# Kernel tuning notes

Hardware: AMD Instinct MI355X
Metric: run time of the kernel (lower is better)

Reference implementation:

```python
import jax, jax.numpy as jnp
import numpy as np

N, E, K = 50000, 1_000_000, 512
C, HALF, L, HID, NT = 64, 32, 16, 1024, 11
EPS = 1e-5


def _bn(x, gamma, beta):
    # BatchNorm1d in training mode: biased batch stats over node axis
    m = x.mean(axis=0)
    v = x.var(axis=0)
    return gamma * (x - m) * jax.lax.rsqrt(v + EPS) + beta


def _biconv(x, src, dst, w, n):
    # adjacency @ x  ->  out_i = sum_{(j->i) in edges} x_j  (edge (src=j, dst=i))
    out = jax.ops.segment_sum(x[src], dst, num_segments=n) @ w[0]
    # adjacency_t @ x -> scatter along src
    back = jax.ops.segment_sum(x[dst], src, num_segments=n) @ w[1]
    return jnp.concatenate([out, back], axis=1)  # [n, C]


def setup_inputs() -> dict:
    key = jax.random.key(0)
    ks = jax.random.split(key, 12)
    return {
        "node_types": jax.random.randint(ks[0], (N,), 0, NT, dtype=jnp.int32),
        "edge_index": jax.random.randint(ks[1], (2, E), 0, N, dtype=jnp.int32),
        "indices": jax.random.randint(ks[2], (K,), 0, N, dtype=jnp.int32),
        "emb": jax.random.normal(ks[3], (NT, C), dtype=jnp.float32),
        "conv0_w": jax.random.normal(ks[4], (2, C, HALF), dtype=jnp.float32) * 0.18,
        "res_bn_gamma": jnp.ones((L, 2, C), dtype=jnp.float32),
        "res_bn_beta": jnp.zeros((L, 2, C), dtype=jnp.float32),
        "res_w": jax.random.normal(ks[5], (L, 2, 2, C, HALF), dtype=jnp.float32) * 0.18,
        "hidden_w": jax.random.normal(ks[6], (18 * C, HID), dtype=jnp.float32) * 0.03,
        "hidden_b": jnp.zeros((HID,), dtype=jnp.float32),
        "out_w": jax.random.normal(ks[7], (HID, 1), dtype=jnp.float32) * 0.03,
        "out_b": jnp.zeros((1,), dtype=jnp.float32),
    }


def reference(node_types, edge_index, indices, emb, conv0_w, res_bn_gamma,
              res_bn_beta, res_w, hidden_w, hidden_b, out_w, out_b):
    n = node_types.shape[0]
    src, dst = edge_index[0], edge_index[1]

    x = emb[node_types]                       # [N, C] embedding lookup
    log0 = x
    x = _biconv(x, src, dst, conv0_w, n)      # conv0
    log1 = x

    def step(x, p):
        gamma, beta, w = p                    # [2,C], [2,C], [2,2,C,HALF]
        skip = x
        h = _bn(jax.nn.relu(x), gamma[0], beta[0])
        h = _biconv(h, src, dst, w[0], n)
        h = _bn(jax.nn.relu(h), gamma[1], beta[1])
        h = _biconv(h, src, dst, w[1], n)
        x = skip + h
        return x, x

    _, ys = jax.lax.scan(step, x, (res_bn_gamma, res_bn_beta, res_w))  # ys [L,N,C]

    full = jnp.concatenate(
        [log0, log1, ys.transpose(1, 0, 2).reshape(n, L * C)], axis=1)  # [N, 18*C]
    sel = full[indices]                        # [K, 18*C]
    h = jax.nn.relu(sel) @ hidden_w + hidden_b
    o = (jax.nn.relu(h) @ out_w + out_b).squeeze(-1)  # [K]
    return jax.nn.softmax(o, axis=0)
```

## Files before the change

### kernel.cpp

```cpp
#include <hip/hip_runtime.h>
#include <hip/hip_bf16.h>

#define NN 50000
#define NE 1000000
#define CC 64
#define LL 16
#define KSEL 512
#define HIDD 1024
#define FULLW 1152
#define EPSV 1e-5f


__global__ __launch_bounds__(256) void hist_kernel(const int* __restrict__ src,
    const int* __restrict__ dst, int* __restrict__ cnt_in, int* __restrict__ cnt_out) {
  int stride = gridDim.x * blockDim.x;
  for (int e = blockIdx.x * blockDim.x + threadIdx.x; e < NE; e += stride) {
    atomicAdd(&cnt_in[dst[e]], 1);
    atomicAdd(&cnt_out[src[e]], 1);
  }
}

__global__ __launch_bounds__(1024) void scan_kernel(const int* __restrict__ cnt,
    int* __restrict__ rp) {
  const int* c = cnt + blockIdx.x * NN;
  int* r = rp + blockIdx.x * (NN + 1);
  __shared__ int part[1024];
  int t = threadIdx.x;
  const int CH = (NN + 1023) / 1024;
  int beg = t * CH;
  int end = min(beg + CH, NN);
  int s = 0;
  for (int i = beg; i < end; ++i) s += c[i];
  part[t] = s;
  __syncthreads();
  if (t == 0) {
    int run = 0;
    for (int i = 0; i < 1024; ++i) { int v = part[i]; part[i] = run; run += v; }
  }
  __syncthreads();
  int off = part[t];
  for (int i = beg; i < end; ++i) { r[i] = off; off += c[i]; }
  if (t == 1023) r[NN] = off;
}

__global__ __launch_bounds__(256) void initcur_kernel(const int* __restrict__ rp_in,
    const int* __restrict__ rp_out, int* __restrict__ cur_in, int* __restrict__ cur_out,
    float* __restrict__ statsA) {
  int i = blockIdx.x * 256 + threadIdx.x;
  if (i < NN) cur_in[i] = rp_in[i];
  else if (i < 2 * NN) cur_out[i - NN] = rp_out[i - NN];
  if (blockIdx.x == 0 && threadIdx.x < 128) statsA[threadIdx.x] = 0.f;
}

__global__ __launch_bounds__(256) void fill_kernel(const int* __restrict__ src,
    const int* __restrict__ dst, int* __restrict__ cur_in, int* __restrict__ cur_out,
    int* __restrict__ col_in, int* __restrict__ col_out) {
  int stride = gridDim.x * blockDim.x;
  for (int e = blockIdx.x * blockDim.x + threadIdx.x; e < NE; e += stride) {
    int s = src[e], d = dst[e];
    int p = atomicAdd(&cur_in[d], 1);
    col_in[p] = s;
    int q = atomicAdd(&cur_out[s], 1);
    col_out[q] = d;
  }
}


__global__ __launch_bounds__(256) void embed_kernel(const int* __restrict__ nt,
    const float* __restrict__ emb, float* __restrict__ X) {
  int id = blockIdx.x * 256 + threadIdx.x;
  if (id >= NN * CC) return;
  X[id] = emb[nt[id >> 6] * CC + (id & 63)];
}

__global__ __launch_bounds__(256) void gather_sel_kernel(const float* __restrict__ xsrc,
    const int* __restrict__ idx, float* __restrict__ sel, int coloff) {
  int tid = blockIdx.x * 256 + threadIdx.x;
  if (tid >= KSEL * CC) return;
  int k = tid >> 6, cch = tid & 63;
  sel[k * FULLW + coloff + cch] = xsrc[idx[k] * CC + cch];
}


__global__ __launch_bounds__(256) void mm_kernel(const float* __restrict__ X,
    __hip_bfloat16* __restrict__ Y, const float* __restrict__ W,
    const float* __restrict__ stats, const float* __restrict__ gamma,
    const float* __restrict__ beta, float* __restrict__ stats_zero) {
  int t = threadIdx.x;
  int lane = t & 63;
  int wid = t >> 6;
  float wreg[CC];
  {
    const float* wb = W + (lane >> 5) * 2048 + (lane & 31);
#pragma unroll
    for (int c2 = 0; c2 < CC; ++c2) wreg[c2] = wb[c2 * 32];
  }
  __shared__ float sc[CC], sh[CC];
  __shared__ __align__(16) float Xs[64][CC];
  if (t < CC) {
    float scale = 1.f, shift = 0.f;
    if (stats) {
      float m = stats[t] * (1.f / NN);
      float v = stats[CC + t] * (1.f / NN) - m * m;
      float is = rsqrtf(v + EPSV);
      scale = gamma[t] * is;
      shift = beta[t] - m * scale;
    }
    sc[t] = scale; sh[t] = shift;
  }
  if (stats_zero && blockIdx.x == 0 && t < 128) stats_zero[t] = 0.f;
  const bool bn = (stats != nullptr);
  for (int row0 = blockIdx.x * 64; row0 < NN; row0 += gridDim.x * 64) {
    int nrows = min(64, NN - row0);
    __syncthreads();
    for (int idx = t; idx < nrows * CC; idx += 256) {
      int r = idx >> 6, cch = idx & 63;
      float v = X[(row0 + r) * CC + cch];
      if (bn) { v = fmaxf(v, 0.f); v = v * sc[cch] + sh[cch]; }
      Xs[r][cch] = v;
    }
    __syncthreads();
    for (int r = wid; r < nrows; r += 4) {
      const float* xr = &Xs[r][0];
      float a0 = 0.f, a1 = 0.f, a2 = 0.f, a3 = 0.f;
#pragma unroll
      for (int c2 = 0; c2 < CC; c2 += 4) {
        float4 xv = *(const float4*)(xr + c2);
        a0 += xv.x * wreg[c2];
        a1 += xv.y * wreg[c2 + 1];
        a2 += xv.z * wreg[c2 + 2];
        a3 += xv.w * wreg[c2 + 3];
      }
      Y[(row0 + r) * CC + lane] = __float2bfloat16((a0 + a1) + (a2 + a3));
    }
  }
}


__global__ __launch_bounds__(256) void seg_kernel(
    const __hip_bfloat16* __restrict__ Y, const float* skip, float* OUT,
    const int* __restrict__ rp_in, const int* __restrict__ col_in,
    const int* __restrict__ rp_out, const int* __restrict__ col_out,
    float* __restrict__ stats_acc) {
  int t = threadIdx.x;
  int c = t & 63;
  int local = t >> 6;
  const int* rp = (c < 32) ? rp_in : rp_out;
  const int* col = (c < 32) ? col_in : col_out;
  float s1 = 0.f, s2 = 0.f;
  for (int i0 = blockIdx.x * 4; i0 < NN; i0 += gridDim.x * 4) {
    int i = i0 + local;
    if (i < NN) {
      int beg = rp[i], end = rp[i + 1];
      float a0 = 0.f, a1 = 0.f, a2 = 0.f, a3 = 0.f;
      float a4 = 0.f, a5 = 0.f, a6 = 0.f, a7 = 0.f;
      int e = beg;
      for (; e + 8 <= end; e += 8) {
        int j0 = col[e], j1 = col[e + 1], j2 = col[e + 2], j3 = col[e + 3];
        int j4 = col[e + 4], j5 = col[e + 5], j6 = col[e + 6], j7 = col[e + 7];
        a0 += __bfloat162float(Y[j0 * CC + c]);
        a1 += __bfloat162float(Y[j1 * CC + c]);
        a2 += __bfloat162float(Y[j2 * CC + c]);
        a3 += __bfloat162float(Y[j3 * CC + c]);
        a4 += __bfloat162float(Y[j4 * CC + c]);
        a5 += __bfloat162float(Y[j5 * CC + c]);
        a6 += __bfloat162float(Y[j6 * CC + c]);
        a7 += __bfloat162float(Y[j7 * CC + c]);
      }
      if (e + 4 <= end) {
        int j0 = col[e], j1 = col[e + 1], j2 = col[e + 2], j3 = col[e + 3];
        a0 += __bfloat162float(Y[j0 * CC + c]);
        a1 += __bfloat162float(Y[j1 * CC + c]);
        a2 += __bfloat162float(Y[j2 * CC + c]);
        a3 += __bfloat162float(Y[j3 * CC + c]);
        e += 4;
      }
      if (e + 2 <= end) {
        int j0 = col[e], j1 = col[e + 1];
        a4 += __bfloat162float(Y[j0 * CC + c]);
        a5 += __bfloat162float(Y[j1 * CC + c]);
        e += 2;
      }
      if (e < end) a6 += __bfloat162float(Y[col[e] * CC + c]);
      float acc = ((a0 + a1) + (a2 + a3)) + ((a4 + a5) + (a6 + a7));
      if (skip) acc += skip[i * CC + c];
      OUT[i * CC + c] = acc;
      float r = fmaxf(acc, 0.f);
      s1 += r; s2 += r * r;
    }
  }
  if (stats_acc) {
    __shared__ float red1[256], red2[256];
    red1[t] = s1; red2[t] = s2;
    __syncthreads();
    if (t < 64) {
      float v1 = red1[t] + red1[t + 64] + red1[t + 128] + red1[t + 192];
      float v2 = red2[t] + red2[t + 64] + red2[t + 128] + red2[t + 192];
      atomicAdd(&stats_acc[t], v1);
      atomicAdd(&stats_acc[CC + t], v2);
    }
  }
}


__global__ __launch_bounds__(64) void hidden_kernel(const float* __restrict__ sel,
    const float* __restrict__ Wh, const float* __restrict__ bh, float* __restrict__ h1) {
  int lane = threadIdx.x;
  int rb = blockIdx.x & 63;
  int jb = blockIdx.x >> 6;
  int j = jb * 64 + lane;
  int r0 = rb * 8;
  float acc[8];
#pragma unroll
  for (int r = 0; r < 8; ++r) acc[r] = 0.f;
  __shared__ __align__(16) float Ss[8][64];
  for (int k0 = 0; k0 < FULLW; k0 += 64) {
    float wreg[64];
#pragma unroll
    for (int c2 = 0; c2 < 64; ++c2) wreg[c2] = Wh[(k0 + c2) * HIDD + j];
    __syncthreads();
#pragma unroll
    for (int r = 0; r < 8; ++r) {
      float v = sel[(r0 + r) * FULLW + k0 + lane];
      Ss[r][lane] = fmaxf(v, 0.f);
    }
    __syncthreads();
#pragma unroll
    for (int r = 0; r < 8; ++r) {
      const float* sr = &Ss[r][0];
      float a0 = 0.f, a1 = 0.f, a2 = 0.f, a3 = 0.f;
#pragma unroll
      for (int c2 = 0; c2 < 64; c2 += 4) {
        float4 sv = *(const float4*)(sr + c2);
        a0 += sv.x * wreg[c2]; a1 += sv.y * wreg[c2 + 1];
        a2 += sv.z * wreg[c2 + 2]; a3 += sv.w * wreg[c2 + 3];
      }
      acc[r] += (a0 + a1) + (a2 + a3);
    }
  }
#pragma unroll
  for (int r = 0; r < 8; ++r) h1[(r0 + r) * HIDD + j] = acc[r] + bh[j];
}

__global__ __launch_bounds__(256) void out_kernel(const float* __restrict__ h1,
    const float* __restrict__ ow, const float* __restrict__ ob, float* __restrict__ logits) {
  int k = blockIdx.x * 4 + (threadIdx.x >> 6);
  int lane = threadIdx.x & 63;
  if (k >= KSEL) return;
  float a = 0.f;
  for (int j = lane; j < HIDD; j += 64) {
    float v = h1[k * HIDD + j];
    a += fmaxf(v, 0.f) * ow[j];
  }
  for (int off = 32; off; off >>= 1) a += __shfl_down(a, off, 64);
  if (lane == 0) logits[k] = a + ob[0];
}

__global__ __launch_bounds__(512) void softmax_kernel(const float* __restrict__ logits,
    float* __restrict__ out) {
  int t = threadIdx.x;
  float v = logits[t];
  __shared__ float red[512];
  red[t] = v;
  __syncthreads();
  for (int s = 256; s; s >>= 1) { if (t < s) red[t] = fmaxf(red[t], red[t + s]); __syncthreads(); }
  float mx = red[0];
  __syncthreads();
  float e = expf(v - mx);
  red[t] = e;
  __syncthreads();
  for (int s = 256; s; s >>= 1) { if (t < s) red[t] += red[t + s]; __syncthreads(); }
  out[t] = e / red[0];
}


extern "C" void kernel_launch(void* const* d_in, const int* in_sizes, int n_in,
                              void* d_out, int out_size, void* d_ws, size_t ws_size,
                              hipStream_t stream) {
  const int* node_types = (const int*)d_in[0];
  const int* edge_index = (const int*)d_in[1];
  const int* indices = (const int*)d_in[2];
  const float* emb = (const float*)d_in[3];
  const float* conv0_w = (const float*)d_in[4];
  const float* bn_g = (const float*)d_in[5];
  const float* bn_b = (const float*)d_in[6];
  const float* res_w = (const float*)d_in[7];
  const float* hw = (const float*)d_in[8];
  const float* hb = (const float*)d_in[9];
  const float* ow = (const float*)d_in[10];
  const float* ob = (const float*)d_in[11];
  float* out = (float*)d_out;
  const int* src = edge_index;
  const int* dst = edge_index + NE;

  char* p = (char*)d_ws;
  size_t off = 0;
  auto alloc = [&](size_t bytes) -> void* {
    void* q = p + off;
    off += (bytes + 255) & ~(size_t)255;
    return q;
  };
  int* cnt = (int*)alloc(2 * NN * sizeof(int));
  int* rp = (int*)alloc(2 * (NN + 1) * sizeof(int));
  int* cur = (int*)alloc(2 * NN * sizeof(int));
  int* col_in = (int*)alloc((size_t)NE * sizeof(int));
  int* col_out = (int*)alloc((size_t)NE * sizeof(int));
  float* X = (float*)alloc((size_t)NN * CC * 4);
  float* H = (float*)alloc((size_t)NN * CC * 4);
  __hip_bfloat16* Y = (__hip_bfloat16*)alloc((size_t)NN * CC * 2);
  float* statsA = (float*)alloc(128 * 4);
  float* statsB = (float*)alloc(128 * 4);
  float* sel = (float*)alloc((size_t)KSEL * FULLW * 4);
  float* h1 = (float*)alloc((size_t)KSEL * HIDD * 4);
  float* logits = (float*)alloc(KSEL * 4);
  (void)ws_size; (void)in_sizes; (void)n_in; (void)out_size;

  int* cnt_in = cnt;  int* cnt_out = cnt + NN;
  int* rp_in = rp;    int* rp_out = rp + NN + 1;
  int* cur_in = cur;  int* cur_out = cur + NN;

  hipMemsetAsync(cnt, 0, 2 * NN * sizeof(int), stream);
  hipLaunchKernelGGL(hist_kernel, dim3(1024), dim3(256), 0, stream, src, dst, cnt_in, cnt_out);
  hipLaunchKernelGGL(scan_kernel, dim3(2), dim3(1024), 0, stream, cnt, rp);
  hipLaunchKernelGGL(initcur_kernel, dim3((2 * NN + 255) / 256), dim3(256), 0, stream,
                     rp_in, rp_out, cur_in, cur_out, statsA);
  hipLaunchKernelGGL(fill_kernel, dim3(1024), dim3(256), 0, stream, src, dst,
                     cur_in, cur_out, col_in, col_out);

  hipLaunchKernelGGL(embed_kernel, dim3((NN * CC + 255) / 256), dim3(256), 0, stream,
                     node_types, emb, X);
  hipLaunchKernelGGL(gather_sel_kernel, dim3(KSEL * CC / 256), dim3(256), 0, stream,
                     X, indices, sel, 0);

  hipLaunchKernelGGL(mm_kernel, dim3(782), dim3(256), 0, stream, X, Y, conv0_w,
                     (const float*)nullptr, (const float*)nullptr, (const float*)nullptr,
                     (float*)nullptr);
  hipLaunchKernelGGL(seg_kernel, dim3(2048), dim3(256), 0, stream, Y, (const float*)nullptr, X,
                     rp_in, col_in, rp_out, col_out, statsA);
  hipLaunchKernelGGL(gather_sel_kernel, dim3(KSEL * CC / 256), dim3(256), 0, stream,
                     X, indices, sel, CC);

  for (int l = 0; l < LL; ++l) {
    const float* w1 = res_w + (size_t)(l * 2 + 0) * 4096;
    const float* w2 = res_w + (size_t)(l * 2 + 1) * 4096;
    const float* g1 = bn_g + (l * 2 + 0) * CC;
    const float* b1 = bn_b + (l * 2 + 0) * CC;
    const float* g2 = bn_g + (l * 2 + 1) * CC;
    const float* b2 = bn_b + (l * 2 + 1) * CC;
    hipLaunchKernelGGL(mm_kernel, dim3(782), dim3(256), 0, stream, X, Y, w1, statsA, g1, b1, statsB);
    hipLaunchKernelGGL(seg_kernel, dim3(2048), dim3(256), 0, stream, Y, (const float*)nullptr, H,
                       rp_in, col_in, rp_out, col_out, statsB);
    hipLaunchKernelGGL(mm_kernel, dim3(782), dim3(256), 0, stream, H, Y, w2, statsB, g2, b2, statsA);
    hipLaunchKernelGGL(seg_kernel, dim3(2048), dim3(256), 0, stream, Y, X, X,
                       rp_in, col_in, rp_out, col_out, statsA);
    hipLaunchKernelGGL(gather_sel_kernel, dim3(KSEL * CC / 256), dim3(256), 0, stream,
                       X, indices, sel, 2 * CC + l * CC);
  }

  hipLaunchKernelGGL(hidden_kernel, dim3(1024), dim3(64), 0, stream, sel, hw, hb, h1);
  hipLaunchKernelGGL(out_kernel, dim3(KSEL / 4), dim3(256), 0, stream, h1, ow, ob, logits);
  hipLaunchKernelGGL(softmax_kernel, dim3(1), dim3(512), 0, stream, logits, out);
}
```

Before: 4.035 ms.

## Parallelize CSR prefix scan, vectorize mm loads, tile hidden layer weights in LDS

Replaces the two-block serial prefix scan with a three-stage multi-block scan that also initializes the cursor array, removing a largely sequential setup kernel. The mm kernel now loads and normalizes input rows as float4 instead of scalars. The hidden-layer kernel uses 256-thread blocks that stage weight and selected-row tiles in shared memory with coalesced float4 loads, replacing the strided per-thread global weight reads. It adds two kernel launches and a temporary buffer in exchange.

Result: faster. 3.677 ms (-8.9%).

```diff
diff --git a/kernel.cpp b/kernel.cpp
--- a/kernel.cpp
+++ b/kernel.cpp
@@ -9,6 +9,7 @@
 #define HIDD 1024
 #define FULLW 1152
 #define EPSV 1e-5f
+#define SBLK 49
 
 
 __global__ __launch_bounds__(256) void hist_kernel(const int* __restrict__ src,
@@ -20,36 +21,57 @@
   }
 }
 
-__global__ __launch_bounds__(1024) void scan_kernel(const int* __restrict__ cnt,
-    int* __restrict__ rp) {
-  const int* c = cnt + blockIdx.x * NN;
-  int* r = rp + blockIdx.x * (NN + 1);
-  __shared__ int part[1024];
-  int t = threadIdx.x;
-  const int CH = (NN + 1023) / 1024;
-  int beg = t * CH;
-  int end = min(beg + CH, NN);
-  int s = 0;
-  for (int i = beg; i < end; ++i) s += c[i];
-  part[t] = s;
+
+__global__ __launch_bounds__(1024) void scan1_kernel(const int* __restrict__ cnt,
+    int* __restrict__ rptmp, int* __restrict__ btot) {
+  int a = blockIdx.x / SBLK, blk = blockIdx.x % SBLK;
+  int t = threadIdx.x;
+  int idx = blk * 1024 + t;
+  int v = (idx < NN) ? cnt[a * NN + idx] : 0;
+  __shared__ int sm[1024];
+  sm[t] = v;
   __syncthreads();
-  if (t == 0) {
-    int run = 0;
-    for (int i = 0; i < 1024; ++i) { int v = part[i]; part[i] = run; run += v; }
-  }
-  __syncthreads();
-  int off = part[t];
-  for (int i = beg; i < end; ++i) { r[i] = off; off += c[i]; }
-  if (t == 1023) r[NN] = off;
-}
-
-__global__ __launch_bounds__(256) void initcur_kernel(const int* __restrict__ rp_in,
-    const int* __restrict__ rp_out, int* __restrict__ cur_in, int* __restrict__ cur_out,
+  for (int off = 1; off < 1024; off <<= 1) {
+    int u = (t >= off) ? sm[t - off] : 0;
+    __syncthreads();
+    sm[t] += u;
+    __syncthreads();
+  }
+  int incl = sm[t];
+  if (idx < NN) rptmp[a * NN + idx] = incl - v;
+  if (t == 1023) btot[a * SBLK + blk] = incl;
+}
+
+__global__ __launch_bounds__(256) void scan2_kernel(int* __restrict__ btot) {
+  __shared__ int sm[256];
+  int t = threadIdx.x;
+  for (int a = 0; a < 2; ++a) {
+    int v = (t < SBLK) ? btot[a * SBLK + t] : 0;
+    sm[t] = v;
+    __syncthreads();
+    for (int off = 1; off < 256; off <<= 1) {
+      int u = (t >= off) ? sm[t - off] : 0;
+      __syncthreads();
+      sm[t] += u;
+      __syncthreads();
+    }
+    if (t < SBLK) btot[a * SBLK + t] = sm[t] - v;
+    __syncthreads();
+  }
+}
+
+__global__ __launch_bounds__(256) void scan3_kernel(const int* __restrict__ rptmp,
+    const int* __restrict__ btot, int* __restrict__ rp, int* __restrict__ cur,
     float* __restrict__ statsA) {
-  int i = blockIdx.x * 256 + threadIdx.x;
-  if (i < NN) cur_in[i] = rp_in[i];
-  else if (i < 2 * NN) cur_out[i - NN] = rp_out[i - NN];
-  if (blockIdx.x == 0 && threadIdx.x < 128) statsA[threadIdx.x] = 0.f;
+  int gid = blockIdx.x * 256 + threadIdx.x;
+  if (gid < 2 * NN) {
+    int a = gid / NN, idx = gid - a * NN;
+    int v = rptmp[gid] + btot[a * SBLK + (idx >> 10)];
+    rp[a * (NN + 1) + idx] = v;
+    cur[gid] = v;
+    if (idx == 0) rp[a * (NN + 1) + NN] = NE;
+  }
+  if (gid < 128) statsA[gid] = 0.f;
 }
 
 __global__ __launch_bounds__(256) void fill_kernel(const int* __restrict__ src,
@@ -113,11 +135,17 @@
   for (int row0 = blockIdx.x * 64; row0 < NN; row0 += gridDim.x * 64) {
     int nrows = min(64, NN - row0);
     __syncthreads();
-    for (int idx = t; idx < nrows * CC; idx += 256) {
-      int r = idx >> 6, cch = idx & 63;
-      float v = X[(row0 + r) * CC + cch];
-      if (bn) { v = fmaxf(v, 0.f); v = v * sc[cch] + sh[cch]; }
-      Xs[r][cch] = v;
+    for (int idx = t; idx < nrows * 16; idx += 256) {
+      int r = idx >> 4, cq = idx & 15;
+      float4 v = *(const float4*)(X + (size_t)(row0 + r) * CC + cq * 4);
+      if (bn) {
+        int c0 = cq * 4;
+        v.x = fmaxf(v.x, 0.f) * sc[c0]     + sh[c0];
+        v.y = fmaxf(v.y, 0.f) * sc[c0 + 1] + sh[c0 + 1];
+        v.z = fmaxf(v.z, 0.f) * sc[c0 + 2] + sh[c0 + 2];
+        v.w = fmaxf(v.w, 0.f) * sc[c0 + 3] + sh[c0 + 3];
+      }
+      *(float4*)&Xs[r][cq * 4] = v;
     }
     __syncthreads();
     for (int r = wid; r < nrows; r += 4) {
@@ -131,7 +159,7 @@
         a2 += xv.z * wreg[c2 + 2];
         a3 += xv.w * wreg[c2 + 3];
       }
-      Y[(row0 + r) * CC + lane] = __float2bfloat16((a0 + a1) + (a2 + a3));
+      Y[(size_t)(row0 + r) * CC + lane] = __float2bfloat16((a0 + a1) + (a2 + a3));
     }
   }
 }
@@ -203,43 +231,54 @@
 }
 
 
-__global__ __launch_bounds__(64) void hidden_kernel(const float* __restrict__ sel,
+__global__ __launch_bounds__(256) void hidden_kernel(const float* __restrict__ sel,
     const float* __restrict__ Wh, const float* __restrict__ bh, float* __restrict__ h1) {
-  int lane = threadIdx.x;
-  int rb = blockIdx.x & 63;
-  int jb = blockIdx.x >> 6;
+  int t = threadIdx.x;
+  int lane = t & 63, w = t >> 6;
+  int jb = blockIdx.x & 15;
+  int rbg = blockIdx.x >> 4;
   int j = jb * 64 + lane;
-  int r0 = rb * 8;
-  float acc[8];
-#pragma unroll
-  for (int r = 0; r < 8; ++r) acc[r] = 0.f;
-  __shared__ __align__(16) float Ss[8][64];
+  int r0 = rbg * 16;
+  __shared__ __align__(16) float Ws[64][64];
+  __shared__ __align__(16) float Ss[16][64];
+  float acc[4] = {0.f, 0.f, 0.f, 0.f};
   for (int k0 = 0; k0 < FULLW; k0 += 64) {
+    __syncthreads();
+    {
+      int col = (t & 15) * 4;
+      int kk = t >> 4;
+#pragma unroll
+      for (int p = 0; p < 4; ++p) {
+        float4 v = *(const float4*)(Wh + (size_t)(k0 + kk + p * 16) * HIDD + jb * 64 + col);
+        *(float4*)&Ws[kk + p * 16][col] = v;
+      }
+      float4 v = *(const float4*)(sel + (size_t)(r0 + kk) * FULLW + k0 + col);
+      v.x = fmaxf(v.x, 0.f); v.y = fmaxf(v.y, 0.f);
+      v.z = fmaxf(v.z, 0.f); v.w = fmaxf(v.w, 0.f);
+      *(float4*)&Ss[kk][col] = v;
+    }
+    __syncthreads();
     float wreg[64];
 #pragma unroll
-    for (int c2 = 0; c2 < 64; ++c2) wreg[c2] = Wh[(k0 + c2) * HIDD + j];
-    __syncthreads();
-#pragma unroll
-    for (int r = 0; r < 8; ++r) {
-      float v = sel[(r0 + r) * FULLW + k0 + lane];
-      Ss[r][lane] = fmaxf(v, 0.f);
-    }
-    __syncthreads();
-#pragma unroll
-    for (int r = 0; r < 8; ++r) {
-      const float* sr = &Ss[r][0];
+    for (int kk = 0; kk < 64; ++kk) wreg[kk] = Ws[kk][lane];
+#pragma unroll
+    for (int rr = 0; rr < 4; ++rr) {
+      const float4* sr = (const float4*)&Ss[w * 4 + rr][0];
       float a0 = 0.f, a1 = 0.f, a2 = 0.f, a3 = 0.f;
 #pragma unroll
-      for (int c2 = 0; c2 < 64; c2 += 4) {
-        float4 sv = *(const float4*)(sr + c2);
-        a0 += sv.x * wreg[c2]; a1 += sv.y * wreg[c2 + 1];
-        a2 += sv.z * wreg[c2 + 2]; a3 += sv.w * wreg[c2 + 3];
-      }
-      acc[r] += (a0 + a1) + (a2 + a3);
-    }
-  }
-#pragma unroll
-  for (int r = 0; r < 8; ++r) h1[(r0 + r) * HIDD + j] = acc[r] + bh[j];
+      for (int kq = 0; kq < 16; ++kq) {
+        float4 sv = sr[kq];
+        a0 += sv.x * wreg[kq * 4];
+        a1 += sv.y * wreg[kq * 4 + 1];
+        a2 += sv.z * wreg[kq * 4 + 2];
+        a3 += sv.w * wreg[kq * 4 + 3];
+      }
+      acc[rr] += (a0 + a1) + (a2 + a3);
+    }
+  }
+#pragma unroll
+  for (int rr = 0; rr < 4; ++rr)
+    h1[(size_t)(r0 + w * 4 + rr) * HIDD + j] = acc[rr] + bh[j];
 }
 
 __global__ __launch_bounds__(256) void out_kernel(const float* __restrict__ h1,
@@ -301,6 +340,8 @@
     return q;
   };
   int* cnt = (int*)alloc(2 * NN * sizeof(int));
+  int* rptmp = (int*)alloc(2 * NN * sizeof(int));
+  int* btot = (int*)alloc(2 * SBLK * sizeof(int));
   int* rp = (int*)alloc(2 * (NN + 1) * sizeof(int));
   int* cur = (int*)alloc(2 * NN * sizeof(int));
   int* col_in = (int*)alloc((size_t)NE * sizeof(int));
@@ -321,9 +362,10 @@
 
   hipMemsetAsync(cnt, 0, 2 * NN * sizeof(int), stream);
   hipLaunchKernelGGL(hist_kernel, dim3(1024), dim3(256), 0, stream, src, dst, cnt_in, cnt_out);
-  hipLaunchKernelGGL(scan_kernel, dim3(2), dim3(1024), 0, stream, cnt, rp);
-  hipLaunchKernelGGL(initcur_kernel, dim3((2 * NN + 255) / 256), dim3(256), 0, stream,
-                     rp_in, rp_out, cur_in, cur_out, statsA);
+  hipLaunchKernelGGL(scan1_kernel, dim3(2 * SBLK), dim3(1024), 0, stream, cnt, rptmp, btot);
+  hipLaunchKernelGGL(scan2_kernel, dim3(1), dim3(256), 0, stream, btot);
+  hipLaunchKernelGGL(scan3_kernel, dim3((2 * NN + 255) / 256), dim3(256), 0, stream,
+                     rptmp, btot, rp, cur, statsA);
   hipLaunchKernelGGL(fill_kernel, dim3(1024), dim3(256), 0, stream, src, dst,
                      cur_in, cur_out, col_in, col_out);
 
@@ -357,7 +399,7 @@
                        X, indices, sel, 2 * CC + l * CC);
   }
 
-  hipLaunchKernelGGL(hidden_kernel, dim3(1024), dim3(64), 0, stream, sel, hw, hb, h1);
+  hipLaunchKernelGGL(hidden_kernel, dim3(512), dim3(256), 0, stream, sel, hw, hb, h1);
   hipLaunchKernelGGL(out_kernel, dim3(KSEL / 4), dim3(256), 0, stream, h1, ow, ob, logits);
   hipLaunchKernelGGL(softmax_kernel, dim3(1), dim3(512), 0, stream, logits, out);
 }
```
